# Performance work log

Measured on AMD Instinct MI355X. Metric: run time of the kernel, lower is better.

Reference implementation:

```python
import jax, jax.numpy as jnp
import numpy as np
from jax import lax

WIN = 7            # win_size -> (7,7,7) window in 3d mode
NPIX = WIN ** 3    # 343
K1, K2 = 0.01, 0.03
COV_NORM = NPIX / (NPIX - 1)
DN = ('NCDHW', 'OIDHW', 'NCDHW')


def _box3d(x):
    """Separable uniform (box) mean filter, VALID padding. Same math as
    conv3d with a ones(wt,ws,ws)/NPIX kernel, but O(win) per voxel per axis."""
    kd = jnp.ones((1, 1, WIN, 1, 1), x.dtype)
    kh = jnp.ones((1, 1, 1, WIN, 1), x.dtype)
    kw = jnp.ones((1, 1, 1, 1, WIN), x.dtype)
    x = lax.conv_general_dilated(x, kd, (1, 1, 1), 'VALID', dimension_numbers=DN)
    x = lax.conv_general_dilated(x, kh, (1, 1, 1), 'VALID', dimension_numbers=DN)
    x = lax.conv_general_dilated(x, kw, (1, 1, 1), 'VALID', dimension_numbers=DN)
    return x / NPIX


def setup_inputs() -> dict:
    key = jax.random.key(0)
    k1, k2, k3 = jax.random.split(key, 3)
    shape = (4, 1, 32, 320, 320)  # [B, C=1, T, H, W]
    pred = jax.random.normal(k1, shape, dtype=jnp.float32)
    targ = jax.random.normal(k2, shape, dtype=jnp.float32)
    data_range = jax.random.uniform(k3, (4,), dtype=jnp.float32)
    return {'pred': pred, 'targ': targ, 'data_range': data_range}


def reference(pred, targ, data_range):
    dr = data_range[:, None, None, None, None].astype(pred.dtype)
    C1 = (K1 * dr) ** 2
    C2 = (K2 * dr) ** 2
    ux = _box3d(pred)
    uy = _box3d(targ)
    uxx = _box3d(pred * pred)
    uyy = _box3d(targ * targ)
    uxy = _box3d(pred * targ)
    vx = COV_NORM * (uxx - ux * ux)
    vy = COV_NORM * (uyy - uy * uy)
    vxy = COV_NORM * (uxy - ux * uy)
    A1 = 2 * ux * uy + C1
    A2 = 2 * vxy + C2
    B1 = ux ** 2 + uy ** 2 + C1
    B2 = vx + vy + C2
    S = (A1 * A2) / (B1 * B2)
    return (1 - S).mean()
```

## Files before the change

### kernel.cpp

```cpp
#include <hip/hip_runtime.h>


#define NPIX 343

constexpr int B = 4, T = 32, H = 320, W = 320;
constexpr int TO = T - 6, HO = H - 6, WO = W - 6;
constexpr long long NOUT = (long long)B * TO * HO * WO;

constexpr int TH = 16, TW = 26;
constexpr int NTH = 20, NTW = 13;
constexpr int OT = 13;
constexpr int NSL = OT + 6;

typedef float v2f __attribute__((ext_vector_type(2)));

template<int N>
__device__ __forceinline__ float row_shr(float x) {
    return __int_as_float(__builtin_amdgcn_update_dpp(
        0, __float_as_int(x), 0x110 | N, 0xF, 0xF, true));
}

__global__ __launch_bounds__(256) void ssim3d_fused(
    const float* __restrict__ pred,
    const float* __restrict__ targ,
    const float* __restrict__ drange,
    double* __restrict__ acc)
{
    __shared__ float4 swv[4][2][10][16];
    __shared__ float wsum[4];

    const int bx = blockIdx.x;
    const int b  = bx / (2 * NTH * NTW);
    int rem      = bx % (2 * NTH * NTW);
    const int half = rem / (NTH * NTW);
    rem          = rem % (NTH * NTW);
    const int h0 = (rem / NTW) * TH;
    const int w0 = (rem % NTW) * TW;
    const int t0 = half * OT;

    const int tid  = threadIdx.x;
    const int wv   = tid >> 6;
    const int lane = tid & 63;
    const int ohl  = lane >> 4;
    const int k    = lane & 15;
    const int h0w  = h0 + 4 * wv;

    const float* pb = pred + (long long)b * T * H * W;
    const float* qb = targ + (long long)b * T * H * W;

    const bool has2 = (lane < 32);
    auto gofs = [&](int i) {
        int r = min(h0w + (i >> 4), H - 1);
        int c = min(w0 + 2 * (i & 15), W - 2);
        return (long long)r * W + c;
    };
    const long long ga0 = gofs(lane);
    const long long ga1 = gofs(lane + 64);
    const long long ga2 = has2 ? gofs(lane + 128) : 0;

    float2 p0, q0, p1, q1, p2, q2;
    auto loadw = [&](int s) {
        const long long so = (long long)(t0 + s) * H * W;
        p0 = *reinterpret_cast<const float2*>(pb + so + ga0);
        q0 = *reinterpret_cast<const float2*>(qb + so + ga0);
        p1 = *reinterpret_cast<const float2*>(pb + so + ga1);
        q1 = *reinterpret_cast<const float2*>(qb + so + ga1);
        if (has2) {
            p2 = *reinterpret_cast<const float2*>(pb + so + ga2);
            q2 = *reinterpret_cast<const float2*>(qb + so + ga2);
        }
    };
    auto commitw = [&](int buf) {
        swv[wv][buf][ohl][k]     = make_float4(p0.x, p0.y, q0.x, q0.y);
        swv[wv][buf][4 + ohl][k] = make_float4(p1.x, p1.y, q1.x, q1.y);
        if (has2)
            swv[wv][buf][8 + ohl][k] = make_float4(p2.x, p2.y, q2.x, q2.y);
    };

    const bool vh = (h0w + ohl < HO);
    const bool k3 = (k >= 3);
    const bool vE = k3 && vh && (w0 + 2 * k - 6 < WO);
    const bool vO = k3 && vh && (w0 + 2 * k - 5 < WO);

    const float dr  = drange[b];
    const float C1s = (0.01f * dr) * (0.01f * dr);
    const float C2s = (0.03f * dr) * (0.03f * dr);
    const float inv  = 1.0f / (float)NPIX;
    const float covn = (float)NPIX / (float)(NPIX - 1);
    const v2f invv  = {inv, inv};
    const v2f C1vv  = {C1s, C1s};
    const v2f C2vv  = {C2s, C2s};
    const v2f covnv = {covn, covn};
    const v2f c2cov = {2.f * covn, 2.f * covn};

    v2f rEO[4][7], tEO[4];
#pragma unroll
    for (int f = 0; f < 4; ++f) {
        tEO[f] = (v2f){0.f, 0.f};
#pragma unroll
        for (int j = 0; j < 7; ++j) rEO[f][j] = (v2f){0.f, 0.f};
    }
    float loss = 0.f;

    auto slice = [&](int s, int jj, bool doEmit, bool doCommit, bool doPrefetch) {
        if (doCommit)  commitw((s + 1) & 1);
        if (doPrefetch) loadw(s + 2);

        const int bs = s & 1;
        v2f c0 = {0.f, 0.f}, c1v = {0.f, 0.f}, c2 = {0.f, 0.f}, c3 = {0.f, 0.f};
#pragma unroll
        for (int dy = 0; dy < 7; ++dy) {
            float4 v = swv[wv][bs][ohl + dy][k];
            v2f vp = {v.x, v.y};
            v2f vq = {v.z, v.w};
            c0 += vp;
            c1v += vq;
            c2 = __builtin_elementwise_fma(vp, vp, c2);
            c2 = __builtin_elementwise_fma(vq, vq, c2);
            c3 = __builtin_elementwise_fma(vp, vq, c3);
        }

        v2f sv[4];
        {
            v2f cf[4] = {c0, c1v, c2, c3};
#pragma unroll
            for (int f = 0; f < 4; ++f) {
                float ps = cf[f].x + cf[f].y;
                float t1 = ps + row_shr<1>(ps);
                float s8 = t1 + row_shr<2>(t1);
                float eL = row_shr<3>(cf[f].x);
                sv[f].x = s8 - cf[f].y;
                sv[f].y = s8 - eL;
            }
        }

#pragma unroll
        for (int f = 0; f < 4; ++f) {
            tEO[f] += sv[f] - rEO[f][jj];
            rEO[f][jj] = sv[f];
        }

        if (doEmit) {
            v2f ux  = tEO[0] * invv;
            v2f uy  = tEO[1] * invv;
            v2f u2  = tEO[2] * invv;
            v2f uxy = tEO[3] * invv;
            v2f m   = __builtin_elementwise_fma(-ux, uy, uxy);
            v2f A2  = __builtin_elementwise_fma(c2cov, m, C2vv);
            v2f nb  = __builtin_elementwise_fma(-ux, ux, u2);
            nb      = __builtin_elementwise_fma(-uy, uy, nb);
            v2f B2  = __builtin_elementwise_fma(covnv, nb, C2vv);
            v2f ux2 = ux + ux;
            v2f A1  = __builtin_elementwise_fma(ux2, uy, C1vv);
            v2f B1  = __builtin_elementwise_fma(
                          ux, ux, __builtin_elementwise_fma(uy, uy, C1vv));
            v2f num = A1 * A2;
            v2f den = B1 * B2;
            float sx = __fdividef(num.x, den.x);
            float sy = __fdividef(num.y, den.y);
            if (vE) loss += 1.f - sx;
            if (vO) loss += 1.f - sy;
        }
    };

    loadw(0);
    commitw(0);
    loadw(1);

#pragma unroll
    for (int jj = 0; jj < 7; ++jj)
        slice(jj, jj, jj == 6, true, true);

#pragma unroll
    for (int jj = 0; jj < 7; ++jj)
        slice(7 + jj, jj, true, true, true);

    slice(14, 0, true, true, true);
    slice(15, 1, true, true, true);
    slice(16, 2, true, true, true);
    slice(17, 3, true, true, false);
    slice(18, 4, true, false, false);

    for (int off = 32; off > 0; off >>= 1)
        loss += __shfl_down(loss, off, 64);
    if (lane == 0) wsum[wv] = loss;
    __syncthreads();
    if (tid == 0) {
        float s = wsum[0] + wsum[1] + wsum[2] + wsum[3];
        atomicAdd(acc, (double)s);
    }
}

__global__ void ssim3d_finalize(const double* __restrict__ acc,
                                float* __restrict__ out)
{
    out[0] = (float)(acc[0] / (double)NOUT);
}

extern "C" void kernel_launch(void* const* d_in, const int* in_sizes, int n_in,
                              void* d_out, int out_size, void* d_ws, size_t ws_size,
                              hipStream_t stream)
{
    const float* pred   = (const float*)d_in[0];
    const float* targ   = (const float*)d_in[1];
    const float* drange = (const float*)d_in[2];
    float* out  = (float*)d_out;
    double* acc = (double*)d_ws;

    hipMemsetAsync(acc, 0, sizeof(double), stream);

    const int nblocks = B * 2 * NTH * NTW;
    ssim3d_fused<<<nblocks, 256, 0, stream>>>(pred, targ, drange, acc);
    ssim3d_finalize<<<1, 1, 0, stream>>>(acc, out);
}
```

Measured before the change: 77.99 us.

## Store temporal ring buffer in packed bf16 to cut registers and raise occupancy

The 7-deep temporal ring of per-slice window sums is now held as packed bf16 pairs instead of fp32 pairs, which halves that register footprint, and launch bounds now request 8 blocks per CU. Address arithmetic moves from 64-bit to 32-bit ints, and the block-level reduction through shared memory and a barrier is replaced by a per-wave atomicAdd. The bf16 rounding of slice sums adds error to the running total, since the value added and later subtracted are both rounded. That error could exceed tolerance, and the atomic traffic on one address grows fourfold.

```diff
diff --git a/kernel.cpp b/kernel.cpp
--- a/kernel.cpp
+++ b/kernel.cpp
@@ -10,7 +10,6 @@
 constexpr int TH = 16, TW = 26;
 constexpr int NTH = 20, NTW = 13;
 constexpr int OT = 13;
-constexpr int NSL = OT + 6;
 
 typedef float v2f __attribute__((ext_vector_type(2)));
 
@@ -20,14 +19,25 @@
         0, __float_as_int(x), 0x110 | N, 0xF, 0xF, true));
 }
 
-__global__ __launch_bounds__(256) void ssim3d_fused(
+__device__ __forceinline__ unsigned pk_bf16(v2f v) {
+    unsigned r;
+    asm("v_cvt_pk_bf16_f32 %0, %1, %2" : "=v"(r) : "v"(v.x), "v"(v.y));
+    return r;
+}
+__device__ __forceinline__ v2f unpk_bf16(unsigned u) {
+    v2f r;
+    r.x = __uint_as_float(u << 16);
+    r.y = __uint_as_float(u & 0xffff0000u);
+    return r;
+}
+
+__global__ __launch_bounds__(256, 8) void ssim3d_fused(
     const float* __restrict__ pred,
     const float* __restrict__ targ,
     const float* __restrict__ drange,
     double* __restrict__ acc)
 {
     __shared__ float4 swv[4][2][10][16];
-    __shared__ float wsum[4];
 
     const int bx = blockIdx.x;
     const int b  = bx / (2 * NTH * NTW);
@@ -45,22 +55,22 @@
     const int k    = lane & 15;
     const int h0w  = h0 + 4 * wv;
 
-    const float* pb = pred + (long long)b * T * H * W;
-    const float* qb = targ + (long long)b * T * H * W;
+    const float* pb = pred + b * (T * H * W);
+    const float* qb = targ + b * (T * H * W);
 
     const bool has2 = (lane < 32);
     auto gofs = [&](int i) {
         int r = min(h0w + (i >> 4), H - 1);
         int c = min(w0 + 2 * (i & 15), W - 2);
-        return (long long)r * W + c;
-    };
-    const long long ga0 = gofs(lane);
-    const long long ga1 = gofs(lane + 64);
-    const long long ga2 = has2 ? gofs(lane + 128) : 0;
+        return r * W + c;
+    };
+    const int ga0 = gofs(lane);
+    const int ga1 = gofs(lane + 64);
+    const int ga2 = has2 ? gofs(lane + 128) : 0;
 
     float2 p0, q0, p1, q1, p2, q2;
     auto loadw = [&](int s) {
-        const long long so = (long long)(t0 + s) * H * W;
+        const int so = (t0 + s) * (H * W);
         p0 = *reinterpret_cast<const float2*>(pb + so + ga0);
         q0 = *reinterpret_cast<const float2*>(qb + so + ga0);
         p1 = *reinterpret_cast<const float2*>(pb + so + ga1);
@@ -93,12 +103,13 @@
     const v2f covnv = {covn, covn};
     const v2f c2cov = {2.f * covn, 2.f * covn};
 
-    v2f rEO[4][7], tEO[4];
+    unsigned rg[4][7];
+    v2f tEO[4];
 #pragma unroll
     for (int f = 0; f < 4; ++f) {
         tEO[f] = (v2f){0.f, 0.f};
 #pragma unroll
-        for (int j = 0; j < 7; ++j) rEO[f][j] = (v2f){0.f, 0.f};
+        for (int j = 0; j < 7; ++j) rg[f][j] = 0u;
     }
     float loss = 0.f;
 
@@ -136,8 +147,11 @@
 
 #pragma unroll
         for (int f = 0; f < 4; ++f) {
-            tEO[f] += sv[f] - rEO[f][jj];
-            rEO[f][jj] = sv[f];
+            unsigned nw = pk_bf16(sv[f]);
+            v2f svr = unpk_bf16(nw);
+            v2f old = unpk_bf16(rg[f][jj]);
+            tEO[f] += svr - old;
+            rg[f][jj] = nw;
         }
 
         if (doEmit) {
@@ -183,12 +197,7 @@
 
     for (int off = 32; off > 0; off >>= 1)
         loss += __shfl_down(loss, off, 64);
-    if (lane == 0) wsum[wv] = loss;
-    __syncthreads();
-    if (tid == 0) {
-        float s = wsum[0] + wsum[1] + wsum[2] + wsum[3];
-        atomicAdd(acc, (double)s);
-    }
+    if (lane == 0) atomicAdd(acc, (double)loss);
 }
 
 __global__ void ssim3d_finalize(const double* __restrict__ acc,
```

Measured after the change: 258.0 us. 3.31x slower.
